# Kernel tuning notes

Measured on AMD Instinct MI355X. Metric: run time of the kernel, lower is better.

Reference implementation:

```python
import jax, jax.numpy as jnp
import numpy as np

DT = 0.001
TAU_MEM = 0.01
TAU_SYN = 0.005
THRESHOLD = 1.0
INITIAL_STATE = 0.0
SS_BETA = 100.0  # SuperSpike surrogate slope (Zenke & Ganguli)


@jax.custom_vjp
def superspike(x):
    # Heaviside spike in forward
    return (x > 0).astype(x.dtype)

def _ss_fwd(x):
    return superspike(x), x

def _ss_bwd(x, g):
    # fast-sigmoid surrogate gradient
    return (g / (SS_BETA * jnp.abs(x) + 1.0) ** 2,)

superspike.defvjp(_ss_fwd, _ss_bwd)


def setup_inputs() -> dict:
    key = jax.random.key(0)
    k1, k2 = jax.random.split(key)
    B, T, IN, OUT = 64, 1024, 256, 256
    inputs = jax.random.normal(k1, (B, T, IN), dtype=jnp.float32)
    w = jax.random.normal(k2, (IN, OUT), dtype=jnp.float32) * 4.0  # scale=4.0 in __init__
    return {"inputs": inputs, "w": w}


def _simulate_mem(inputs, w):
    # inputs: [B, T, IN], w: [IN, OUT]
    x = jnp.matmul(inputs, w)  # [B, T, OUT]
    T = x.shape[1]
    dcy_mem = jnp.exp(jnp.asarray(-DT / (TAU_MEM + 1e-16), dtype=x.dtype))
    scl_mem = 1.0 - dcy_mem
    dcy_syn = jnp.exp(jnp.asarray(-DT / (TAU_SYN + 1e-16), dtype=x.dtype))

    zeros0 = jnp.zeros_like(x[:, 0])  # initial_state = 0

    def step(carry, x_t):
        syn, mem = carry
        new_syn = dcy_syn * syn + x_t
        new_mem = dcy_mem * mem + scl_mem * syn  # uses OLD syn
        out = superspike(mem - THRESHOLD)        # spike from OLD mem
        new_mem = new_mem * (1.0 - out)          # reset
        return (new_syn, new_mem), new_mem

    # loop runs over t = 0 .. T-2 (matches `for t in range(nb_steps - 1)`)
    xs = jnp.swapaxes(x[:, : T - 1], 0, 1)  # [T-1, B, OUT]
    _, mems = jax.lax.scan(step, (zeros0, zeros0), xs)
    mems = jnp.swapaxes(mems, 0, 1)  # [B, T-1, OUT]
    # prepend the initial stored state (zeros, since initial_state=0)
    U = jnp.concatenate([zeros0[:, None, :], mems], axis=1)  # [B, T, OUT]
    return U


def reference(inputs, w):
    # monitor == 'mem' -> return membrane potential trace U
    return _simulate_mem(inputs, w)
```

## Files before the change

### kernel.cpp

```cpp
#include <hip/hip_runtime.h>
#include <cmath>

typedef short bf16x8 __attribute__((ext_vector_type(8)));
typedef float f32x4 __attribute__((ext_vector_type(4)));
typedef unsigned short us8v __attribute__((ext_vector_type(8)));

#define T_DIM 1024

__device__ __forceinline__ unsigned short rtn_bf16(float f) {
    unsigned u = __float_as_uint(f);
    return (unsigned short)((u + 0x7FFFu + ((u >> 16) & 1u)) >> 16);
}
__device__ __forceinline__ float bf_to_f(unsigned short h) {
    return __uint_as_float(((unsigned)h) << 16);
}
__device__ __forceinline__ void split3(float f, unsigned short& h1,
                                       unsigned short& h2, unsigned short& h3) {
    unsigned u = __float_as_uint(f);
    h1 = (unsigned short)(u >> 16);
    float r1 = f - __uint_as_float(u & 0xFFFF0000u);
    unsigned u1 = __float_as_uint(r1);
    h2 = (unsigned short)(u1 >> 16);
    float r2 = r1 - __uint_as_float(u1 & 0xFFFF0000u);
    h3 = rtn_bf16(r2);
}

__global__ __launch_bounds__(256) void lif_wsplit(const float* __restrict__ w,
                                                  unsigned short* __restrict__ wT1,
                                                  unsigned short* __restrict__ wT2,
                                                  unsigned short* __restrict__ wT3) {
    const int id = blockIdx.x * 256 + threadIdx.x;
    const int k = id >> 8, n = id & 255;
    unsigned short h1, h2, h3;
    split3(w[id], h1, h2, h3);
    const int o = n * 256 + k;
    wT1[o] = h1; wT2[o] = h2; wT3[o] = h3;
}

__global__ __launch_bounds__(256) void lif_gemm_mfma(const float* __restrict__ in,
                                                     const unsigned short* __restrict__ wT1,
                                                     const unsigned short* __restrict__ wT2,
                                                     const unsigned short* __restrict__ wT3,
                                                     float* __restrict__ xbuf) {
    __shared__ unsigned short As[3][128 * 32];

    const int tid  = threadIdx.x;
    const int bm   = blockIdx.x;
    const int bn   = blockIdx.y;
    const int wave = tid >> 6;
    const int lane = tid & 63;
    const int l15  = lane & 15;
    const int quad = lane >> 4;
    const int wm   = (wave >> 1) * 64;
    const int wn   = (wave & 1) * 64;

    f32x4 acc[4][4];
    #pragma unroll
    for (int i = 0; i < 4; ++i)
        #pragma unroll
        for (int j = 0; j < 4; ++j) acc[i][j] = (f32x4){0.f, 0.f, 0.f, 0.f};

    const int r  = tid >> 1;
    const int hf = tid & 1;
    const int rx = r & 3;
    const float* arow = in + (size_t)(bm * 128 + r) * 256 + hf * 16;

    for (int kt = 0; kt < 8; ++kt) {
        const int k0 = kt * 32;
        float4 av[4];
        #pragma unroll
        for (int j = 0; j < 4; ++j)
            av[j] = *(const float4*)(arow + k0 + j * 4);

        __syncthreads();
        #pragma unroll
        for (int j2 = 0; j2 < 2; ++j2) {
            const float fv[8] = {av[2*j2].x, av[2*j2].y, av[2*j2].z, av[2*j2].w,
                                 av[2*j2+1].x, av[2*j2+1].y, av[2*j2+1].z, av[2*j2+1].w};
            us8v o1, o2, o3;
            #pragma unroll
            for (int i = 0; i < 8; ++i) {
                unsigned short h1, h2, h3;
                split3(fv[i], h1, h2, h3);
                o1[i] = h1; o2[i] = h2; o3[i] = h3;
            }
            const int cp = ((hf * 2 + j2) ^ rx) * 8;
            *(us8v*)&As[0][r * 32 + cp] = o1;
            *(us8v*)&As[1][r * 32 + cp] = o2;
            *(us8v*)&As[2][r * 32 + cp] = o3;
        }
        __syncthreads();

        bf16x8 af[3][4];
        #pragma unroll
        for (int mt = 0; mt < 4; ++mt) {
            const int m  = wm + mt * 16 + l15;
            const int ro = m * 32 + ((quad ^ (m & 3)) * 8);
            af[0][mt] = *(const bf16x8*)&As[0][ro];
            af[1][mt] = *(const bf16x8*)&As[1][ro];
            af[2][mt] = *(const bf16x8*)&As[2][ro];
        }

        size_t wo = (size_t)(bn * 128 + wn + l15) * 256 + k0 + quad * 8;
        bf16x8 b1 = *(const bf16x8*)(wT1 + wo);
        bf16x8 b2 = *(const bf16x8*)(wT2 + wo);
        bf16x8 b3 = *(const bf16x8*)(wT3 + wo);

        #pragma unroll
        for (int nt = 0; nt < 4; ++nt) {
            bf16x8 n1, n2, n3;
            if (nt < 3) {
                const size_t won = wo + (size_t)16 * 256;
                n1 = *(const bf16x8*)(wT1 + won);
                n2 = *(const bf16x8*)(wT2 + won);
                n3 = *(const bf16x8*)(wT3 + won);
            }
            #pragma unroll
            for (int mt = 0; mt < 4; ++mt) {
                f32x4 a = acc[mt][nt];
                a = __builtin_amdgcn_mfma_f32_16x16x32_bf16(af[0][mt], b1, a, 0, 0, 0);
                a = __builtin_amdgcn_mfma_f32_16x16x32_bf16(af[0][mt], b2, a, 0, 0, 0);
                a = __builtin_amdgcn_mfma_f32_16x16x32_bf16(af[1][mt], b1, a, 0, 0, 0);
                a = __builtin_amdgcn_mfma_f32_16x16x32_bf16(af[1][mt], b2, a, 0, 0, 0);
                a = __builtin_amdgcn_mfma_f32_16x16x32_bf16(af[0][mt], b3, a, 0, 0, 0);
                a = __builtin_amdgcn_mfma_f32_16x16x32_bf16(af[2][mt], b1, a, 0, 0, 0);
                acc[mt][nt] = a;
            }
            if (nt < 3) { b1 = n1; b2 = n2; b3 = n3; wo += (size_t)16 * 256; }
        }
    }

    #pragma unroll
    for (int mt = 0; mt < 4; ++mt) {
        #pragma unroll
        for (int nt = 0; nt < 4; ++nt) {
            const int C  = bn * 128 + wn + nt * 16 + l15;
            const int Rb = bm * 128 + wm + mt * 16 + quad * 4;
            #pragma unroll
            for (int reg = 0; reg < 4; ++reg)
                xbuf[(size_t)(Rb + reg) * 256 + C] = acc[mt][nt][reg];
        }
    }
}

__global__ __launch_bounds__(64, 1) void lif_scan(const float* __restrict__ xbuf,
                                                  float* __restrict__ U,
                                                  double dcy_syn, double dcy_mem,
                                                  double scl_mem) {
    const int b = blockIdx.x >> 2;
    const int o = (blockIdx.x & 3) * 64 + threadIdx.x;

    const float* xp = xbuf + (size_t)b * T_DIM * 256 + o;
    float* up = U + (size_t)b * T_DIM * 256 + o;

    up[0] = 0.0f;
    double syn = 0.0, mem = 0.0;

    float bufA[32], bufB[32];
    #pragma unroll
    for (int j = 0; j < 32; ++j)
        bufA[j] = __builtin_nontemporal_load(xp + (size_t)j * 256);

    #pragma unroll 1
    for (int bt = 0; bt < 16; ++bt) {
        const int tb = bt * 64;
        {
            const float* np = xp + (size_t)(tb + 32) * 256;
            #pragma unroll
            for (int j = 0; j < 32; ++j)
                bufB[j] = __builtin_nontemporal_load(np + (size_t)j * 256);
        }
        #pragma unroll
        for (int j = 0; j < 32; ++j) {
            const int t = tb + j;
            double nm = dcy_mem * mem + scl_mem * syn;
            if (mem - 1.0 > 0.0) nm = 0.0;
            syn = dcy_syn * syn + (double)bufA[j];
            mem = nm;
            up[(size_t)(t + 1) * 256] = (float)mem;
        }
        if (bt < 15) {
            const float* np = xp + (size_t)(tb + 64) * 256;
            #pragma unroll
            for (int j = 0; j < 32; ++j)
                bufA[j] = __builtin_nontemporal_load(np + (size_t)j * 256);
        }
        #pragma unroll
        for (int j = 0; j < 32; ++j) {
            const int t = tb + 32 + j;
            double nm = dcy_mem * mem + scl_mem * syn;
            if (mem - 1.0 > 0.0) nm = 0.0;
            syn = dcy_syn * syn + (double)bufB[j];
            mem = nm;
            if (t < T_DIM - 1)
                up[(size_t)(t + 1) * 256] = (float)mem;
        }
    }
}

extern "C" void kernel_launch(void* const* d_in, const int* in_sizes, int n_in,
                              void* d_out, int out_size, void* d_ws, size_t ws_size,
                              hipStream_t stream) {
    const float* in = (const float*)d_in[0];
    const float* w  = (const float*)d_in[1];
    float* U = (float*)d_out;

    const double dcy_mem = exp(-0.001 / (0.01  + 1e-16));
    const double dcy_syn = exp(-0.001 / (0.005 + 1e-16));
    const double scl_mem = 1.0 - dcy_mem;

    char* ws = (char*)d_ws;
    unsigned short* wT1 = (unsigned short*)ws;
    unsigned short* wT2 = (unsigned short*)(ws + 131072);
    unsigned short* wT3 = (unsigned short*)(ws + 262144);
    float* xbuf = (float*)(ws + 524288);

    lif_wsplit<<<dim3(256), dim3(256), 0, stream>>>(w, wT1, wT2, wT3);
    lif_gemm_mfma<<<dim3(512, 2), dim3(256), 0, stream>>>(in, wT1, wT2, wT3, xbuf);
    lif_scan<<<dim3(256), dim3(64), 0, stream>>>(xbuf, U, dcy_syn, dcy_mem, scl_mem);
}
```

Baseline: 192.9 us.

## Double-buffer GEMM A tiles in LDS and deepen scan prefetch with nontemporal stores

The GEMM now keeps two LDS buffers for the split bf16 A tile and prefetches global A one tile ahead, so there is one barrier per k-step and the split work overlaps the MFMA loop. The scan kernel doubles its register prefetch depth from 32 to 64 timesteps per buffer and writes outputs with nontemporal stores. The aim is to hide global load latency in both kernels. In exchange, LDS use doubles and scan register pressure rises.

```diff
diff --git a/kernel.cpp b/kernel.cpp
--- a/kernel.cpp
+++ b/kernel.cpp
@@ -23,6 +23,24 @@
     h2 = (unsigned short)(u1 >> 16);
     float r2 = r1 - __uint_as_float(u1 & 0xFFFF0000u);
     h3 = rtn_bf16(r2);
+}
+
+__device__ __forceinline__ void split_store8(const float4& a, const float4& b,
+                                             unsigned short* __restrict__ A0,
+                                             unsigned short* __restrict__ A1,
+                                             unsigned short* __restrict__ A2,
+                                             int off) {
+    const float fv[8] = {a.x, a.y, a.z, a.w, b.x, b.y, b.z, b.w};
+    us8v o1, o2, o3;
+    #pragma unroll
+    for (int i = 0; i < 8; ++i) {
+        unsigned short h1, h2, h3;
+        split3(fv[i], h1, h2, h3);
+        o1[i] = h1; o2[i] = h2; o3[i] = h3;
+    }
+    *(us8v*)&A0[off] = o1;
+    *(us8v*)&A1[off] = o2;
+    *(us8v*)&A2[off] = o3;
 }
 
 __global__ __launch_bounds__(256) void lif_wsplit(const float* __restrict__ w,
@@ -42,7 +60,7 @@
                                                      const unsigned short* __restrict__ wT2,
                                                      const unsigned short* __restrict__ wT3,
                                                      float* __restrict__ xbuf) {
-    __shared__ unsigned short As[3][128 * 32];
+    __shared__ unsigned short As[2][3][128 * 32];
 
     const int tid  = threadIdx.x;
     const int bm   = blockIdx.x;
@@ -63,44 +81,50 @@
     const int r  = tid >> 1;
     const int hf = tid & 1;
     const int rx = r & 3;
+    const int off0 = r * 32 + (((hf << 1) | 0) ^ rx) * 8;
+    const int off1 = r * 32 + (((hf << 1) | 1) ^ rx) * 8;
     const float* arow = in + (size_t)(bm * 128 + r) * 256 + hf * 16;
 
+    float4 av0[4];
+    #pragma unroll
+    for (int j = 0; j < 4; ++j) av0[j] = *(const float4*)(arow + j * 4);
+    float4 avn[4];
+    #pragma unroll
+    for (int j = 0; j < 4; ++j) avn[j] = *(const float4*)(arow + 32 + j * 4);
+    split_store8(av0[0], av0[1], &As[0][0][0], &As[0][1][0], &As[0][2][0], off0);
+    split_store8(av0[2], av0[3], &As[0][0][0], &As[0][1][0], &As[0][2][0], off1);
+    __syncthreads();
+
+    #pragma unroll
     for (int kt = 0; kt < 8; ++kt) {
-        const int k0 = kt * 32;
-        float4 av[4];
-        #pragma unroll
-        for (int j = 0; j < 4; ++j)
-            av[j] = *(const float4*)(arow + k0 + j * 4);
-
-        __syncthreads();
-        #pragma unroll
-        for (int j2 = 0; j2 < 2; ++j2) {
-            const float fv[8] = {av[2*j2].x, av[2*j2].y, av[2*j2].z, av[2*j2].w,
-                                 av[2*j2+1].x, av[2*j2+1].y, av[2*j2+1].z, av[2*j2+1].w};
-            us8v o1, o2, o3;
-            #pragma unroll
-            for (int i = 0; i < 8; ++i) {
-                unsigned short h1, h2, h3;
-                split3(fv[i], h1, h2, h3);
-                o1[i] = h1; o2[i] = h2; o3[i] = h3;
-            }
-            const int cp = ((hf * 2 + j2) ^ rx) * 8;
-            *(us8v*)&As[0][r * 32 + cp] = o1;
-            *(us8v*)&As[1][r * 32 + cp] = o2;
-            *(us8v*)&As[2][r * 32 + cp] = o3;
-        }
-        __syncthreads();
+        const int cur = kt & 1;
 
         bf16x8 af[3][4];
         #pragma unroll
         for (int mt = 0; mt < 4; ++mt) {
             const int m  = wm + mt * 16 + l15;
             const int ro = m * 32 + ((quad ^ (m & 3)) * 8);
-            af[0][mt] = *(const bf16x8*)&As[0][ro];
-            af[1][mt] = *(const bf16x8*)&As[1][ro];
-            af[2][mt] = *(const bf16x8*)&As[2][ro];
-        }
-
+            af[0][mt] = *(const bf16x8*)&As[cur][0][ro];
+            af[1][mt] = *(const bf16x8*)&As[cur][1][ro];
+            af[2][mt] = *(const bf16x8*)&As[cur][2][ro];
+        }
+
+        if (kt < 7) {
+            split_store8(avn[0], avn[1], &As[cur ^ 1][0][0], &As[cur ^ 1][1][0],
+                         &As[cur ^ 1][2][0], off0);
+            split_store8(avn[2], avn[3], &As[cur ^ 1][0][0], &As[cur ^ 1][1][0],
+                         &As[cur ^ 1][2][0], off1);
+        }
+
+        __syncthreads();
+
+        if (kt < 6) {
+            const float* ap = arow + (kt + 2) * 32;
+            #pragma unroll
+            for (int j = 0; j < 4; ++j) avn[j] = *(const float4*)(ap + j * 4);
+        }
+
+        const int k0 = kt * 32;
         size_t wo = (size_t)(bn * 128 + wn + l15) * 256 + k0 + quad * 8;
         bf16x8 b1 = *(const bf16x8*)(wT1 + wo);
         bf16x8 b2 = *(const bf16x8*)(wT2 + wo);
@@ -156,44 +180,44 @@
     up[0] = 0.0f;
     double syn = 0.0, mem = 0.0;
 
-    float bufA[32], bufB[32];
-    #pragma unroll
-    for (int j = 0; j < 32; ++j)
+    float bufA[64], bufB[64];
+    #pragma unroll
+    for (int j = 0; j < 64; ++j)
         bufA[j] = __builtin_nontemporal_load(xp + (size_t)j * 256);
 
     #pragma unroll 1
-    for (int bt = 0; bt < 16; ++bt) {
-        const int tb = bt * 64;
+    for (int bt = 0; bt < 8; ++bt) {
+        const int tb = bt * 128;
         {
-            const float* np = xp + (size_t)(tb + 32) * 256;
-            #pragma unroll
-            for (int j = 0; j < 32; ++j)
+            const float* np = xp + (size_t)(tb + 64) * 256;
+            #pragma unroll
+            for (int j = 0; j < 64; ++j)
                 bufB[j] = __builtin_nontemporal_load(np + (size_t)j * 256);
         }
         #pragma unroll
-        for (int j = 0; j < 32; ++j) {
+        for (int j = 0; j < 64; ++j) {
             const int t = tb + j;
             double nm = dcy_mem * mem + scl_mem * syn;
             if (mem - 1.0 > 0.0) nm = 0.0;
             syn = dcy_syn * syn + (double)bufA[j];
             mem = nm;
-            up[(size_t)(t + 1) * 256] = (float)mem;
-        }
-        if (bt < 15) {
-            const float* np = xp + (size_t)(tb + 64) * 256;
-            #pragma unroll
-            for (int j = 0; j < 32; ++j)
+            __builtin_nontemporal_store((float)mem, up + (size_t)(t + 1) * 256);
+        }
+        if (bt < 7) {
+            const float* np = xp + (size_t)(tb + 128) * 256;
+            #pragma unroll
+            for (int j = 0; j < 64; ++j)
                 bufA[j] = __builtin_nontemporal_load(np + (size_t)j * 256);
         }
         #pragma unroll
-        for (int j = 0; j < 32; ++j) {
-            const int t = tb + 32 + j;
+        for (int j = 0; j < 64; ++j) {
+            const int t = tb + 64 + j;
             double nm = dcy_mem * mem + scl_mem * syn;
             if (mem - 1.0 > 0.0) nm = 0.0;
             syn = dcy_syn * syn + (double)bufB[j];
             mem = nm;
             if (t < T_DIM - 1)
-                up[(size_t)(t + 1) * 256] = (float)mem;
+                __builtin_nontemporal_store((float)mem, up + (size_t)(t + 1) * 256);
         }
     }
 }
```

New measurement: 189.6 us. About the same (-1.7%).
